# Performance work log

Measured on AMD Instinct MI355X. Metric: run time of the kernel, lower is better.

## Reference

```python
import jax, jax.numpy as jnp
import numpy as np

B, S, DIM = 4, 4096, 4096
HD, RD = 512, 64          # head_dim, rope_head_dim
RATIO, COFF = 4, 2        # compress_ratio=4 -> overlap -> coff=2
EPS = 1e-6
BLOCK_SIZE = 64
N_COMP = S // RATIO       # compressed slots per sequence
N_BLOCKS = B * N_COMP // BLOCK_SIZE


def setup_inputs() -> dict:
    key = jax.random.key(0)
    ks = jax.random.split(key, 6)
    x = jax.random.normal(ks[0], (B, S, DIM), jnp.float32)
    wkv_w = jax.random.normal(ks[1], (DIM, COFF * HD), jnp.float32) * 0.02
    wgate_w = jax.random.normal(ks[2], (DIM, COFF * HD), jnp.float32) * 0.02
    ape = jax.random.normal(ks[3], (RATIO, COFF * HD), jnp.float32) * 0.02
    norm_w = jnp.ones((HD,), jnp.float32)
    # RoPE table for compressed positions: token t uses compressed pos t//RATIO
    pos = jnp.arange(S)
    inv = 1.0 / (10000.0 ** (jnp.arange(0, RD, 2, dtype=jnp.float32) / RD))
    ang = (pos // RATIO).astype(jnp.float32)[:, None] * inv[None, :]  # [S, RD//2]
    cos, sin = jnp.cos(ang), jnp.sin(ang)
    block_offsets = jnp.arange(N_BLOCKS, dtype=jnp.int32).reshape(B, -1)
    start_pos = jnp.zeros((B,), jnp.int32)  # pure prefill: ring-buffer state empty
    return dict(x=x, wkv_w=wkv_w, wgate_w=wgate_w, ape=ape, norm_w=norm_w,
                cos=cos, sin=sin, block_offsets=block_offsets, start_pos=start_pos)


def _compress(x, wkv_w, wgate_w, ape, norm_w, cos, sin):
    kv = x @ wkv_w                      # [B,S,COFF*HD]
    sc = x @ wgate_w                    # [B,S,COFF*HD]
    # sliding window of RATIO tokens ending at each token (ring-buffer semantics,
    # start_pos=0 so the whole window lives in the current chunk)
    idx = jnp.arange(S)[:, None] - (RATIO - 1) + jnp.arange(RATIO)[None, :]  # [S,RATIO]
    valid = idx >= 0
    idxc = jnp.clip(idx, 0, S - 1)
    kv_w = kv[:, idxc]                  # [B,S,RATIO,COFF*HD]
    sc_w = sc[:, idxc]
    ape_w = ape[idxc % RATIO]           # [S,RATIO,COFF*HD] (ape by pos % ratio)
    sc_w = jnp.where(valid[None, :, :, None], sc_w, -jnp.inf)
    w = jax.nn.softmax(sc_w, axis=2)    # score-gated compression over the window
    out = jnp.sum(w * (kv_w + ape_w[None]), axis=2)  # [B,S,COFF*HD]
    out = out[..., :HD] + out[..., HD:]              # fold overlapping halves
    # RMSNorm over head_dim
    var = jnp.mean(out * out, axis=-1, keepdims=True)
    ckv = out * jax.lax.rsqrt(var + EPS) * norm_w
    # RoPE (complex/interleaved) on last RD channels
    r = ckv[..., -RD:].reshape(B, S, RD // 2, 2)
    cr, ci = r[..., 0], r[..., 1]
    c, s = cos[None], sin[None]         # [1,S,RD//2]
    rot = jnp.stack([cr * c - ci * s, cr * s + ci * c], axis=-1).reshape(B, S, RD)
    return jnp.concatenate([ckv[..., :-RD], rot], axis=-1)  # [B,S,HD]


def reference(x, wkv_w, wgate_w, ape, norm_w, cos, sin, block_offsets, start_pos):
    ckv = _compress(x, wkv_w, wgate_w, ape, norm_w, cos, sin)
    ckv_flat = ckv.reshape(B * S, HD)
    # fill_compressed_kv: one compressed row per RATIO tokens -> paged block cache
    sel = ckv[:, RATIO - 1::RATIO]                   # [B, N_COMP, HD]
    cidx = jnp.arange(N_COMP)
    blk = block_offsets[:, cidx // BLOCK_SIZE]       # [B, N_COMP]
    off = jnp.tile(cidx % BLOCK_SIZE, B)
    cache = jnp.zeros((N_BLOCKS, BLOCK_SIZE, HD), jnp.float32)
    cache = cache.at[blk.reshape(-1), off].set(sel.reshape(-1, HD))
    return ckv_flat, cache
```

## Files before the change

### kernel.cpp

```cpp
#include <hip/hip_runtime.h>

#define BATCH 4
#define SLEN  4096
#define DIMK  4096
#define HD    512
#define RD    64
#define NCOLS 2048
#define MROWS (BATCH*SLEN)

typedef __attribute__((ext_vector_type(8))) short bf16x8;
typedef __attribute__((ext_vector_type(4))) float f32x4;
typedef unsigned short u16;

__device__ inline u16 f2b(float f) {
  union { float f; unsigned u; } x; x.f = f;
  unsigned r = (x.u + 0x7fffu + ((x.u >> 16) & 1u)) >> 16;
  return (u16)r;
}
__device__ inline float b2f(u16 u) {
  union { float f; unsigned u; } x; x.u = ((unsigned)u) << 16; return x.f;
}

#define GLL16(gp, lp) __builtin_amdgcn_global_load_lds( \
    (__attribute__((address_space(1))) void*)(gp),      \
    (__attribute__((address_space(3))) void*)(lp), 16, 0, 0)

__global__ __launch_bounds__(256) void cvt_x_kernel(const float4* __restrict__ x,
                                                    u16* __restrict__ xb) {
  size_t i = (size_t)blockIdx.x * 256 + threadIdx.x;
  float4 a = x[2 * i], b = x[2 * i + 1];
  bf16x8 v;
  v[0] = (short)f2b(a.x); v[1] = (short)f2b(a.y);
  v[2] = (short)f2b(a.z); v[3] = (short)f2b(a.w);
  v[4] = (short)f2b(b.x); v[5] = (short)f2b(b.y);
  v[6] = (short)f2b(b.z); v[7] = (short)f2b(b.w);
  *(bf16x8*)(xb + i * 8) = v;
}

__global__ __launch_bounds__(256) void build_wt_kernel(const float* __restrict__ wkv,
                                                       const float* __restrict__ wg,
                                                       u16* __restrict__ Wt) {
  __shared__ u16 tile[64][72];
  const int n0 = blockIdx.x * 64;
  const int k0 = blockIdx.y * 64;
  const float* src = (n0 < 1024) ? wkv : wg;
  const int nbase = (n0 < 1024) ? n0 : (n0 - 1024);
  const int t = threadIdx.x;
  const int nn = t & 63, kq = t >> 6;
  #pragma unroll
  for (int j = 0; j < 16; ++j) {
    int k = kq + j * 4;
    float v = src[(size_t)(k0 + k) * 1024 + nbase + nn];
    tile[nn][k] = f2b(v);
  }
  __syncthreads();
  const int kk8 = (t & 7) * 8;
  #pragma unroll
  for (int j = 0; j < 2; ++j) {
    int nn2 = (t >> 3) + j * 32;
    bf16x8 v = *(bf16x8*)&tile[nn2][kk8];
    *(bf16x8*)&Wt[(size_t)(n0 + nn2) * DIMK + k0 + kk8] = v;
  }
}

__global__ __launch_bounds__(512, 2) void gemm_kernel(const u16* __restrict__ A,
                                                      const u16* __restrict__ Bt,
                                                      u16* __restrict__ C) {
  __shared__ __align__(16) u16 Asm[2][8][256][8];
  __shared__ __align__(16) u16 Bsm[2][8][256][8];
  const int t = threadIdx.x;
  const int lane = t & 63, wave = t >> 6;

  const int orig = blockIdx.x;
  const int lid = (orig & 7) * 64 + (orig >> 3);
  const int mt = lid >> 3, nt = lid & 7;
  const int m0 = mt * 256, n0 = nt * 256;
  const int wr = wave >> 2, wc = wave & 3;

  f32x4 acc[8][4] = {};

  const int rowS = t & 255, kcS = t >> 8;
  const u16* gA = A  + (size_t)(m0 + rowS) * DIMK;
  const u16* gB = Bt + (size_t)(n0 + rowS) * DIMK;

#define SA(buf, tt, kh) do {                                                  \
    GLL16(gA + (tt) * 64 + (kh) * 32 + kcS * 8,                               \
          &Asm[buf][(kh) * 4 + kcS][rowS][0]);                                \
    GLL16(gA + (tt) * 64 + (kh) * 32 + (2 + kcS) * 8,                         \
          &Asm[buf][(kh) * 4 + 2 + kcS][rowS][0]);                            \
  } while (0)
#define SB(buf, tt, kh) do {                                                  \
    GLL16(gB + (tt) * 64 + (kh) * 32 + kcS * 8,                               \
          &Bsm[buf][(kh) * 4 + kcS][rowS][0]);                                \
    GLL16(gB + (tt) * 64 + (kh) * 32 + (2 + kcS) * 8,                         \
          &Bsm[buf][(kh) * 4 + 2 + kcS][rowS][0]);                            \
  } while (0)

#define MFMA16(mb) do {                                                       \
    __builtin_amdgcn_s_setprio(1);                                            \
    _Pragma("unroll")                                                         \
    for (int m = 0; m < 4; ++m) {                                             \
      _Pragma("unroll")                                                       \
      for (int n = 0; n < 4; ++n)                                             \
        acc[(mb) + m][n] = __builtin_amdgcn_mfma_f32_16x16x32_bf16(           \
            af[m], bf[n], acc[(mb) + m][n], 0, 0, 0);                         \
    }                                                                         \
    __builtin_amdgcn_s_setprio(0);                                            \
  } while (0)

#define BARF()  do { asm volatile("s_barrier" ::: "memory");                  \
                     __builtin_amdgcn_sched_barrier(0); } while (0)
#define LKW0()  asm volatile("s_waitcnt lgkmcnt(0)" ::: "memory")
#define VMW(n)  asm volatile("s_waitcnt vmcnt(" #n ")" ::: "memory")

  const int fr = lane & 15, fk = lane >> 4;
  const int NT = DIMK / 64;

  SA(0, 0, 0); SB(0, 0, 0); SA(0, 0, 1); SB(0, 0, 1);
  SA(1, 1, 0); SB(1, 1, 0);
  VMW(8);
  BARF();

  bf16x8 af[4], bf[4];

  for (int tt = 0; tt < NT; ++tt) {
    const int c = tt & 1;
    const int t1 = (tt + 1 < NT) ? tt + 1 : NT - 1;
    const int t2 = (tt + 2 < NT) ? tt + 2 : NT - 1;

    SA(c ^ 1, t1, 1);
    #pragma unroll
    for (int m = 0; m < 4; ++m)
      af[m] = *(const bf16x8*)&Asm[c][fk][wr * 128 + m * 16 + fr][0];
    #pragma unroll
    for (int n = 0; n < 4; ++n)
      bf[n] = *(const bf16x8*)&Bsm[c][fk][wc * 64 + n * 16 + fr][0];
    LKW0();
    BARF();
    MFMA16(0);

    SB(c ^ 1, t1, 1);
    #pragma unroll
    for (int m = 0; m < 4; ++m)
      af[m] = *(const bf16x8*)&Asm[c][fk][wr * 128 + (m + 4) * 16 + fr][0];
    LKW0();
    VMW(8);
    BARF();
    MFMA16(4);

    SA(c, t2, 0);
    #pragma unroll
    for (int m = 0; m < 4; ++m)
      af[m] = *(const bf16x8*)&Asm[c][4 + fk][wr * 128 + m * 16 + fr][0];
    #pragma unroll
    for (int n = 0; n < 4; ++n)
      bf[n] = *(const bf16x8*)&Bsm[c][4 + fk][wc * 64 + n * 16 + fr][0];
    LKW0();
    BARF();
    MFMA16(0);

    SB(c, t2, 0);
    #pragma unroll
    for (int m = 0; m < 4; ++m)
      af[m] = *(const bf16x8*)&Asm[c][4 + fk][wr * 128 + (m + 4) * 16 + fr][0];
    LKW0();
    VMW(8);
    BARF();
    MFMA16(4);
  }
  VMW(0);
#undef SA
#undef SB
#undef MFMA16
#undef BARF
#undef LKW0
#undef VMW

  const int fq = lane >> 4;
  #pragma unroll
  for (int m = 0; m < 8; ++m) {
    #pragma unroll
    for (int n = 0; n < 4; ++n) {
      int col = n0 + wc * 64 + n * 16 + fr;
      int rowb = m0 + wr * 128 + m * 16 + fq * 4;
      #pragma unroll
      for (int j = 0; j < 4; ++j)
        C[(size_t)(rowb + j) * NCOLS + col] = f2b(acc[m][n][j]);
    }
  }
}

__device__ inline float soft_half(const bf16x8* scv, const bf16x8* kvv,
                                  const float ap[4][8], const bool valid[4], int i) {
  float sc[4];
  #pragma unroll
  for (int r = 0; r < 4; ++r)
    sc[r] = valid[r] ? b2f((u16)scv[r][i]) : -1e30f;
  float m = fmaxf(fmaxf(sc[0], sc[1]), fmaxf(sc[2], sc[3]));
  float e[4], sum = 0.f;
  #pragma unroll
  for (int r = 0; r < 4; ++r) { e[r] = __expf(sc[r] - m); sum += e[r]; }
  float inv = 1.0f / sum;
  float o = 0.f;
  #pragma unroll
  for (int r = 0; r < 4; ++r)
    o += e[r] * (b2f((u16)kvv[r][i]) + ap[r][i]);
  return o * inv;
}

__global__ __launch_bounds__(256) void fuse_kernel(const u16* __restrict__ kvsc,
                                                   const float* __restrict__ ape,
                                                   const float* __restrict__ norm_w,
                                                   const float* __restrict__ cosb,
                                                   const float* __restrict__ sinb,
                                                   const int* __restrict__ bo,
                                                   float* __restrict__ ckv_out,
                                                   float* __restrict__ cache_out) {
  __shared__ float ape_s[4][1024];
  const int t = threadIdx.x;
  for (int j = t; j < 1024; j += 256)
    ((float4*)&ape_s[0][0])[j] = ((const float4*)ape)[j];
  __syncthreads();

  const int wave = t >> 6, lane = t & 63;
  const int g = blockIdx.x * 4 + wave;
  const int b = g >> 12, s = g & 4095;
  const int c0 = lane * 8;

  const u16* base = kvsc + (size_t)b * SLEN * NCOLS;
  bf16x8 kv_lo[4], kv_hi[4], sc_lo[4], sc_hi[4];
  float apl[4][8], aph[4][8];
  bool valid[4];
  #pragma unroll
  for (int r = 0; r < 4; ++r) {
    int sr = s - 3 + r;
    valid[r] = (sr >= 0);
    int src = sr < 0 ? 0 : sr;
    int rot = src & 3;
    const u16* rp = base + (size_t)src * NCOLS;
    kv_lo[r] = *(const bf16x8*)(rp + c0);
    kv_hi[r] = *(const bf16x8*)(rp + 512 + c0);
    sc_lo[r] = *(const bf16x8*)(rp + 1024 + c0);
    sc_hi[r] = *(const bf16x8*)(rp + 1536 + c0);
    *(float4*)&apl[r][0] = *(const float4*)&ape_s[rot][c0];
    *(float4*)&apl[r][4] = *(const float4*)&ape_s[rot][c0 + 4];
    *(float4*)&aph[r][0] = *(const float4*)&ape_s[rot][512 + c0];
    *(float4*)&aph[r][4] = *(const float4*)&ape_s[rot][512 + c0 + 4];
  }

  float res[8];
  float sumsq = 0.f;
  #pragma unroll
  for (int i = 0; i < 8; ++i) {
    float o = soft_half(sc_lo, kv_lo, apl, valid, i) +
              soft_half(sc_hi, kv_hi, aph, valid, i);
    res[i] = o;
    sumsq += o * o;
  }
  #pragma unroll
  for (int off = 32; off > 0; off >>= 1)
    sumsq += __shfl_xor(sumsq, off, 64);
  const float scale = rsqrtf(sumsq * (1.0f / 512.0f) + 1e-6f);

  float4 nwa = *(const float4*)&norm_w[c0];
  float4 nwb = *(const float4*)&norm_w[c0 + 4];
  res[0] *= scale * nwa.x; res[1] *= scale * nwa.y;
  res[2] *= scale * nwa.z; res[3] *= scale * nwa.w;
  res[4] *= scale * nwb.x; res[5] *= scale * nwb.y;
  res[6] *= scale * nwb.z; res[7] *= scale * nwb.w;

  if (lane >= 56) {
    int j0 = (lane - 56) * 4;
    float4 cs = *(const float4*)&cosb[(size_t)s * 32 + j0];
    float4 sn = *(const float4*)&sinb[(size_t)s * 32 + j0];
    float cc[4] = {cs.x, cs.y, cs.z, cs.w};
    float ss[4] = {sn.x, sn.y, sn.z, sn.w};
    #pragma unroll
    for (int p = 0; p < 4; ++p) {
      float cr = res[2 * p], ci = res[2 * p + 1];
      res[2 * p]     = cr * cc[p] - ci * ss[p];
      res[2 * p + 1] = cr * ss[p] + ci * cc[p];
    }
  }

  float4 v0 = make_float4(res[0], res[1], res[2], res[3]);
  float4 v1 = make_float4(res[4], res[5], res[6], res[7]);
  float* op = ckv_out + (size_t)g * HD + c0;
  *(float4*)op = v0;
  *(float4*)(op + 4) = v1;

  if ((s & 3) == 3) {
    int cidx = s >> 2;
    int blk = bo[b * 16 + (cidx >> 6)];
    int off = cidx & 63;
    float* cp = cache_out + ((size_t)blk * 64 + off) * HD + c0;
    *(float4*)cp = v0;
    *(float4*)(cp + 4) = v1;
  }
}

extern "C" void kernel_launch(void* const* d_in, const int* in_sizes, int n_in,
                              void* d_out, int out_size, void* d_ws, size_t ws_size,
                              hipStream_t stream) {
  const float* x    = (const float*)d_in[0];
  const float* wkv  = (const float*)d_in[1];
  const float* wg   = (const float*)d_in[2];
  const float* ape  = (const float*)d_in[3];
  const float* nw   = (const float*)d_in[4];
  const float* cosb = (const float*)d_in[5];
  const float* sinb = (const float*)d_in[6];
  const int*   bo   = (const int*)d_in[7];

  float* out = (float*)d_out;
  char* ws = (char*)d_ws;
  u16* xb   = (u16*)ws;
  u16* Wt   = (u16*)(ws + (size_t)MROWS * DIMK * 2);
  u16* kvsc = (u16*)(ws + (size_t)MROWS * DIMK * 2 + (size_t)NCOLS * DIMK * 2);

  hipLaunchKernelGGL(cvt_x_kernel, dim3(32768), dim3(256), 0, stream,
                     (const float4*)x, xb);
  hipLaunchKernelGGL(build_wt_kernel, dim3(32, 64), dim3(256), 0, stream, wkv, wg, Wt);
  hipLaunchKernelGGL(gemm_kernel, dim3(512), dim3(512), 0, stream, xb, Wt, kvsc);

  float* ckv_out = out;
  float* cache_out = out + (size_t)MROWS * HD;
  hipMemsetAsync(cache_out, 0, (size_t)64 * 64 * HD * sizeof(float), stream);
  hipLaunchKernelGGL(fuse_kernel, dim3(MROWS / 4), dim3(256), 0, stream,
                     kvsc, ape, nw, cosb, sinb, bo, ckv_out, cache_out);
}
```

Before: 517.5 us.

## Switch GEMM to triple-buffered K=32 stages with XOR-swizzled row-major LDS

The bf16 GEMM's shared-memory staging moves from a double-buffered, k-chunk-major layout (K=64 per iteration) to a triple-buffered, row-major [256][32] layout with K=32 per iteration. The 16-byte column chunk index is XOR-swizzled by row bits to avoid LDS bank conflicts. Loads are issued two stages ahead, with the vmcnt wait changed to match. The aim is deeper prefetch and conflict-free LDS reads, at the cost of twice as many loop iterations and barriers per K.

New measurement: 509.4 us. No clear change (-1.6%).

```diff
diff --git a/kernel.cpp b/kernel.cpp
--- a/kernel.cpp
+++ b/kernel.cpp
@@ -66,8 +66,8 @@
 __global__ __launch_bounds__(512, 2) void gemm_kernel(const u16* __restrict__ A,
                                                       const u16* __restrict__ Bt,
                                                       u16* __restrict__ C) {
-  __shared__ __align__(16) u16 Asm[2][8][256][8];
-  __shared__ __align__(16) u16 Bsm[2][8][256][8];
+  __shared__ __align__(16) u16 Asm[3][256][32];
+  __shared__ __align__(16) u16 Bsm[3][256][32];
   const int t = threadIdx.x;
   const int lane = t & 63, wave = t >> 6;
 
@@ -79,22 +79,19 @@
 
   f32x4 acc[8][4] = {};
 
-  const int rowS = t & 255, kcS = t >> 8;
-  const u16* gA = A  + (size_t)(m0 + rowS) * DIMK;
-  const u16* gB = Bt + (size_t)(n0 + rowS) * DIMK;
-
-#define SA(buf, tt, kh) do {                                                  \
-    GLL16(gA + (tt) * 64 + (kh) * 32 + kcS * 8,                               \
-          &Asm[buf][(kh) * 4 + kcS][rowS][0]);                                \
-    GLL16(gA + (tt) * 64 + (kh) * 32 + (2 + kcS) * 8,                         \
-          &Asm[buf][(kh) * 4 + 2 + kcS][rowS][0]);                            \
-  } while (0)
-#define SB(buf, tt, kh) do {                                                  \
-    GLL16(gB + (tt) * 64 + (kh) * 32 + kcS * 8,                               \
-          &Bsm[buf][(kh) * 4 + kcS][rowS][0]);                                \
-    GLL16(gB + (tt) * 64 + (kh) * 32 + (2 + kcS) * 8,                         \
-          &Bsm[buf][(kh) * 4 + 2 + kcS][rowS][0]);                            \
-  } while (0)
+  const int rowT = t >> 2, colT = t & 3;
+  const int colX = colT ^ (rowT & 3) ^ ((rowT >> 2) & 3);
+  const u16* gA0 = A  + (size_t)(m0 + rowT) * DIMK + colX * 8;
+  const u16* gB0 = Bt + (size_t)(n0 + rowT) * DIMK + colX * 8;
+  u16* AsmF = &Asm[0][0][0];
+  u16* BsmF = &Bsm[0][0][0];
+  u16* lA0 = AsmF + rowT * 32 + colT * 8;
+  u16* lB0 = BsmF + rowT * 32 + colT * 8;
+
+#define SA(buf, tt, h) GLL16(gA0 + (size_t)((h) * 128) * DIMK + (tt) * 32, \
+                             lA0 + (buf) * 8192 + (h) * 4096)
+#define SB(buf, tt, h) GLL16(gB0 + (size_t)((h) * 128) * DIMK + (tt) * 32, \
+                             lB0 + (buf) * 8192 + (h) * 4096)
 
 #define MFMA16(mb) do {                                                       \
     __builtin_amdgcn_s_setprio(1);                                            \
@@ -111,70 +108,49 @@
 #define BARF()  do { asm volatile("s_barrier" ::: "memory");                  \
                      __builtin_amdgcn_sched_barrier(0); } while (0)
 #define LKW0()  asm volatile("s_waitcnt lgkmcnt(0)" ::: "memory")
-#define VMW(n)  asm volatile("s_waitcnt vmcnt(" #n ")" ::: "memory")
 
   const int fr = lane & 15, fk = lane >> 4;
-  const int NT = DIMK / 64;
-
-  SA(0, 0, 0); SB(0, 0, 0); SA(0, 0, 1); SB(0, 0, 1);
-  SA(1, 1, 0); SB(1, 1, 0);
-  VMW(8);
+  const int fkx = (fk ^ (fr & 3) ^ ((fr >> 2) & 3)) * 8;
+  const int NT = DIMK / 32;
+
+  SA(0, 0, 0); SA(0, 0, 1); SB(0, 0, 0); SB(0, 0, 1);
+  SA(1, 1, 0); SA(1, 1, 1); SB(1, 1, 0); SB(1, 1, 1);
+  asm volatile("s_waitcnt vmcnt(4)" ::: "memory");
   BARF();
 
   bf16x8 af[4], bf[4];
 
   for (int tt = 0; tt < NT; ++tt) {
-    const int c = tt & 1;
-    const int t1 = (tt + 1 < NT) ? tt + 1 : NT - 1;
-    const int t2 = (tt + 2 < NT) ? tt + 2 : NT - 1;
-
-    SA(c ^ 1, t1, 1);
+    const int cb = tt % 3;
+    const int wb = (tt + 2) % 3;
+    const bool st = (tt + 2 < NT);
+
+    if (st) { SA(wb, tt + 2, 0); SA(wb, tt + 2, 1); }
     #pragma unroll
     for (int m = 0; m < 4; ++m)
-      af[m] = *(const bf16x8*)&Asm[c][fk][wr * 128 + m * 16 + fr][0];
+      af[m] = *(const bf16x8*)(AsmF + cb * 8192 + (wr * 128 + m * 16 + fr) * 32 + fkx);
     #pragma unroll
     for (int n = 0; n < 4; ++n)
-      bf[n] = *(const bf16x8*)&Bsm[c][fk][wc * 64 + n * 16 + fr][0];
+      bf[n] = *(const bf16x8*)(BsmF + cb * 8192 + (wc * 64 + n * 16 + fr) * 32 + fkx);
     LKW0();
     BARF();
     MFMA16(0);
 
-    SB(c ^ 1, t1, 1);
+    if (st) { SB(wb, tt + 2, 0); SB(wb, tt + 2, 1); }
     #pragma unroll
     for (int m = 0; m < 4; ++m)
-      af[m] = *(const bf16x8*)&Asm[c][fk][wr * 128 + (m + 4) * 16 + fr][0];
+      af[m] = *(const bf16x8*)(AsmF + cb * 8192 + (wr * 128 + (m + 4) * 16 + fr) * 32 + fkx);
     LKW0();
-    VMW(8);
+    if (tt < NT - 2) asm volatile("s_waitcnt vmcnt(4)" ::: "memory");
+    else             asm volatile("s_waitcnt vmcnt(0)" ::: "memory");
     BARF();
     MFMA16(4);
-
-    SA(c, t2, 0);
-    #pragma unroll
-    for (int m = 0; m < 4; ++m)
-      af[m] = *(const bf16x8*)&Asm[c][4 + fk][wr * 128 + m * 16 + fr][0];
-    #pragma unroll
-    for (int n = 0; n < 4; ++n)
-      bf[n] = *(const bf16x8*)&Bsm[c][4 + fk][wc * 64 + n * 16 + fr][0];
-    LKW0();
-    BARF();
-    MFMA16(0);
-
-    SB(c, t2, 0);
-    #pragma unroll
-    for (int m = 0; m < 4; ++m)
-      af[m] = *(const bf16x8*)&Asm[c][4 + fk][wr * 128 + (m + 4) * 16 + fr][0];
-    LKW0();
-    VMW(8);
-    BARF();
-    MFMA16(4);
-  }
-  VMW(0);
+  }
 #undef SA
 #undef SB
 #undef MFMA16
 #undef BARF
 #undef LKW0
-#undef VMW
 
   const int fq = lane >> 4;
   #pragma unroll
```
